# Kernel optimization log

Hardware: AMD Instinct MI355X
Metric: run time of the kernel (lower is better)

## Reference

```python
import jax, jax.numpy as jnp
import numpy as np

DEPTH = 7  # leaves = 2**(DEPTH-1) = 64

def setup_inputs() -> dict:
    key = jax.random.key(0)
    k1, k2, k3 = jax.random.split(key, 3)
    bs, dimx, dimy = 32768, 2048, 2048
    leaves = 2 ** (DEPTH - 1)
    x = jax.random.normal(k1, (bs, dimx), dtype=jnp.float32)
    w = 0.1 * jax.random.uniform(k2, (dimx, leaves - 1), dtype=jnp.float32)
    b = jnp.zeros((leaves - 1,), dtype=jnp.float32)
    responses = 0.1 * jax.random.uniform(k3, (leaves, dimy), dtype=jnp.float32)
    return {"x": x, "w": w, "b": b, "responses": responses}

def reference(x, w, b, responses):
    bs = x.shape[0]
    # gate probabilities for all internal nodes of the binary tree: [bs, leaves-1]
    gate = jax.nn.sigmoid(x @ w + b)
    running = jnp.ones((bs, 1), dtype=x.dtype)
    for i in range(1, DEPTH):
        parents = gate[:, 2 ** (i - 1) - 1: 2 ** i - 1]  # [bs, 2**(i-1)]
        # torch.stack([left, right], dim=1).reshape -> [left | right] concat order
        running = jnp.concatenate([parents * running, (1.0 - parents) * running], axis=1)
    return running @ responses  # [bs, dimy]
```

## Files before the change

### kernel.cpp

```cpp
#include <hip/hip_runtime.h>
#include <hip/hip_bf16.h>


typedef short bf16x8 __attribute__((ext_vector_type(8)));
typedef float f32x4  __attribute__((ext_vector_type(4)));

#define BS    32768
#define DIMX  2048
#define NODES 63
#define NL    64
#define DIMY  2048

__device__ __forceinline__ unsigned short f2bf(float f) {
    union { float f; unsigned int u; } v; v.f = f;
    unsigned int r = v.u + 0x7FFFu + ((v.u >> 16) & 1u);
    return (unsigned short)(r >> 16);
}
__device__ __forceinline__ float bf2f(unsigned short h) {
    union { float f; unsigned int u; } v; v.u = ((unsigned int)h) << 16;
    return v.f;
}

__global__ __launch_bounds__(256) void prep(const float* __restrict__ w,
                                            const float* __restrict__ R,
                                            unsigned short* __restrict__ wFs,
                                            unsigned short* __restrict__ RTs) {
    int f = blockIdx.x * 256 + threadIdx.x;
    if (f < 262144) {
        int e   = f & 7;
        int l   = (f >> 3) & 63;
        int hl  = (f >> 9) & 1;
        int g16 = (f >> 10) & 3;
        int kk  = (f >> 12) & 1;
        int k   = f >> 13;
        int n    = g16 * 16 + (l & 15);
        int kcol = k * 64 + kk * 32 + (l >> 4) * 8 + e;
        float v = (n < NODES) ? w[(size_t)kcol * NODES + n] : 0.0f;
        unsigned short h = f2bf(v);
        wFs[f] = hl ? f2bf(v - bf2f(h)) : h;
    } else {
        int f2 = f - 262144;
        int e  = f2 & 7;
        int l  = (f2 >> 3) & 63;
        int kh = (f2 >> 9) & 1;
        int nf = f2 >> 10;
        int k  = kh * 32 + (l >> 4) * 8 + e;
        int n  = nf * 16 + (l & 15);
        RTs[f2] = f2bf(R[(size_t)k * DIMY + n]);
    }
}

#define GBM   32
#define GBK   64
#define GLD   72
#define NSTEP (DIMX / GBK)

__device__ __forceinline__ bf16x8 pack8(float4 a, float4 b) {
    union { __hip_bfloat162 h2[4]; bf16x8 v; } u;
    u.h2[0] = __float22bfloat162_rn(make_float2(a.x, a.y));
    u.h2[1] = __float22bfloat162_rn(make_float2(a.z, a.w));
    u.h2[2] = __float22bfloat162_rn(make_float2(b.x, b.y));
    u.h2[3] = __float22bfloat162_rn(make_float2(b.z, b.w));
    return u.v;
}

__global__ __launch_bounds__(256, 6) void fused_kernel(const float* __restrict__ x,
                                                       const unsigned short* __restrict__ wFs,
                                                       const float* __restrict__ bias,
                                                       const unsigned short* __restrict__ RTs,
                                                       float* __restrict__ out) {
    __shared__ __align__(16) unsigned short xs[GBM][GLD];
    __shared__ float gl[GBM][NL + 1];

    const int t    = threadIdx.x;
    const int lane = t & 63;
    const int wv   = t >> 6;
    const int lr   = lane & 15;
    const int lg   = lane >> 4;
    const int m0   = blockIdx.x * GBM;
    const int rm   = wv & 1;
    const int cfp  = wv >> 1;

    const int xr = t >> 3;
    const int xc = (t & 7) * 8;
    const float* xsrc = x + (size_t)(m0 + xr) * DIMX + xc;

    const unsigned short* wb = wFs + (size_t)lane * 8;
    #define WFRAG(k, kk, ci, hl) \
        (*(const bf16x8*)(wb + (size_t)((((k) * 2 + (kk)) * 4 + (cfp * 2 + (ci))) * 2 + (hl)) * 512))

    float4 rx0 = *(const float4*)(xsrc);
    float4 rx1 = *(const float4*)(xsrc + 4);

    f32x4 acc[2];
    acc[0] = (f32x4){0.f, 0.f, 0.f, 0.f};
    acc[1] = (f32x4){0.f, 0.f, 0.f, 0.f};

    for (int k = 0; k < NSTEP; ++k) {
        __syncthreads();
        *(bf16x8*)&xs[xr][xc] = pack8(rx0, rx1);
        __syncthreads();
        if (k + 1 < NSTEP) {
            const int ko = (k + 1) * GBK;
            rx0 = *(const float4*)(xsrc + ko);
            rx1 = *(const float4*)(xsrc + ko + 4);
        }
        #pragma unroll
        for (int kk = 0; kk < 2; ++kk) {
            bf16x8 a = *(const bf16x8*)&xs[rm * 16 + lr][kk * 32 + lg * 8];
            #pragma unroll
            for (int ci = 0; ci < 2; ++ci) {
                bf16x8 bh = WFRAG(k, kk, ci, 0);
                bf16x8 bo = WFRAG(k, kk, ci, 1);
                acc[ci] = __builtin_amdgcn_mfma_f32_16x16x32_bf16(a, bh, acc[ci], 0, 0, 0);
                acc[ci] = __builtin_amdgcn_mfma_f32_16x16x32_bf16(a, bo, acc[ci], 0, 0, 0);
            }
        }
    }
    #undef WFRAG

    #pragma unroll
    for (int ci = 0; ci < 2; ++ci) {
        const int col = cfp * 32 + ci * 16 + lr;
        const float bb = bias[col < NODES ? col : 0];
        #pragma unroll
        for (int i = 0; i < 4; ++i) {
            int row = rm * 16 + lg * 4 + i;
            float s = acc[ci][i] + bb;
            gl[row][col] = 1.0f / (1.0f + __expf(-s));
        }
    }
    __syncthreads();

    {
        const int rr  = t >> 3;
        const int sub = t & 7;
        const int b5 = sub & 1, b4 = (sub >> 1) & 1, mh = sub >> 2;
        const float* g = gl[rr];
        float a2[2], a4[4], a8[8];
        float g0 = g[0];
        a2[0] = g0; a2[1] = 1.f - g0;
        #pragma unroll
        for (int m = 0; m < 4; ++m) {
            float gg = g[1 + (m & 1)];
            a4[m] = a2[m & 1] * ((m & 2) ? (1.f - gg) : gg);
        }
        #pragma unroll
        for (int m = 0; m < 8; ++m) {
            float gg = g[3 + (m & 3)];
            a8[m] = a4[m & 3] * ((m & 4) ? (1.f - gg) : gg);
        }
        unsigned short o[8];
        #pragma unroll
        for (int j = 0; j < 8; ++j) {
            int m = mh * 8 + j;
            float g4 = g[7 + j];
            float p  = a8[j] * (mh ? (1.f - g4) : g4);
            float g5 = g[15 + m];
            p *= b4 ? (1.f - g5) : g5;
            float g6 = g[31 + m + 16 * b4];
            p *= b5 ? (1.f - g6) : g6;
            o[j] = f2bf(p);
        }
        uint4 q;
        q.x = (unsigned)o[0] | ((unsigned)o[1] << 16);
        q.y = (unsigned)o[2] | ((unsigned)o[3] << 16);
        q.z = (unsigned)o[4] | ((unsigned)o[5] << 16);
        q.w = (unsigned)o[6] | ((unsigned)o[7] << 16);
        *(uint4*)&xs[rr][b5 * 32 + b4 * 16 + mh * 8] = q;
    }
    __syncthreads();

    bf16x8 pa[2][2];
    #pragma unroll
    for (int rf = 0; rf < 2; ++rf)
        #pragma unroll
        for (int kh = 0; kh < 2; ++kh)
            pa[rf][kh] = *(const bf16x8*)&xs[rf * 16 + lr][kh * 32 + lg * 8];

    const unsigned short* bbase = RTs + (size_t)(wv * 4) * 512 + (size_t)lane * 8;
    #define BLD(s, ci, kh) (*(const bf16x8*)(bbase + (size_t)(((s) * 16 + (ci) * 2 + (kh))) * 512))

    bf16x8 cur[4], nxt[4];
    cur[0] = BLD(0, 0, 0); cur[1] = BLD(0, 0, 1);
    cur[2] = BLD(0, 1, 0); cur[3] = BLD(0, 1, 1);

    float* op = out + (size_t)(m0 + lg * 4) * DIMY + wv * 32 + lr;

    #pragma unroll
    for (int s = 0; s < 16; ++s) {
        if (s + 1 < 16) {
            nxt[0] = BLD(s + 1, 0, 0); nxt[1] = BLD(s + 1, 0, 1);
            nxt[2] = BLD(s + 1, 1, 0); nxt[3] = BLD(s + 1, 1, 1);
        }
        f32x4 oa[2][2];
        #pragma unroll
        for (int rf = 0; rf < 2; ++rf)
            #pragma unroll
            for (int ci = 0; ci < 2; ++ci) {
                oa[rf][ci] = (f32x4){0.f, 0.f, 0.f, 0.f};
                oa[rf][ci] = __builtin_amdgcn_mfma_f32_16x16x32_bf16(pa[rf][0], cur[ci * 2 + 0],
                                                                     oa[rf][ci], 0, 0, 0);
                oa[rf][ci] = __builtin_amdgcn_mfma_f32_16x16x32_bf16(pa[rf][1], cur[ci * 2 + 1],
                                                                     oa[rf][ci], 0, 0, 0);
            }
        #pragma unroll
        for (int rf = 0; rf < 2; ++rf)
            #pragma unroll
            for (int ci = 0; ci < 2; ++ci)
                #pragma unroll
                for (int i = 0; i < 4; ++i)
                    op[(size_t)(rf * 16 + i) * DIMY + s * 128 + ci * 16] = oa[rf][ci][i];
        #pragma unroll
        for (int q = 0; q < 4; ++q) cur[q] = nxt[q];
    }
    #undef BLD
}

extern "C" void kernel_launch(void* const* d_in, const int* in_sizes, int n_in,
                              void* d_out, int out_size, void* d_ws, size_t ws_size,
                              hipStream_t stream) {
    const float* x = (const float*)d_in[0];
    const float* w = (const float*)d_in[1];
    const float* b = (const float*)d_in[2];
    const float* R = (const float*)d_in[3];
    float* out = (float*)d_out;

    char* ws = (char*)d_ws;
    unsigned short* wFs = (unsigned short*)ws;
    unsigned short* RTs = (unsigned short*)(ws + 524288);

    prep<<<dim3(1536), 256, 0, stream>>>(w, R, wFs, RTs);
    fused_kernel<<<dim3(BS / GBM), 256, 0, stream>>>(x, wFs, b, RTs, out);
}
```

Baseline: 155.7 us.

## Halve row tile to 16 per block and raise occupancy target

```diff
diff --git a/kernel.cpp b/kernel.cpp
--- a/kernel.cpp
+++ b/kernel.cpp
@@ -50,21 +50,12 @@
     }
 }
 
-#define GBM   32
+#define GBM   16
 #define GBK   64
 #define GLD   72
 #define NSTEP (DIMX / GBK)
 
-__device__ __forceinline__ bf16x8 pack8(float4 a, float4 b) {
-    union { __hip_bfloat162 h2[4]; bf16x8 v; } u;
-    u.h2[0] = __float22bfloat162_rn(make_float2(a.x, a.y));
-    u.h2[1] = __float22bfloat162_rn(make_float2(a.z, a.w));
-    u.h2[2] = __float22bfloat162_rn(make_float2(b.x, b.y));
-    u.h2[3] = __float22bfloat162_rn(make_float2(b.z, b.w));
-    return u.v;
-}
-
-__global__ __launch_bounds__(256, 6) void fused_kernel(const float* __restrict__ x,
+__global__ __launch_bounds__(256, 8) void fused_kernel(const float* __restrict__ x,
                                                        const unsigned short* __restrict__ wFs,
                                                        const float* __restrict__ bias,
                                                        const unsigned short* __restrict__ RTs,
@@ -78,64 +69,56 @@
     const int lr   = lane & 15;
     const int lg   = lane >> 4;
     const int m0   = blockIdx.x * GBM;
-    const int rm   = wv & 1;
-    const int cfp  = wv >> 1;
-
-    const int xr = t >> 3;
-    const int xc = (t & 7) * 8;
+
+    const int xr = t >> 4;
+    const int xc = (t & 15) * 4;
     const float* xsrc = x + (size_t)(m0 + xr) * DIMX + xc;
 
     const unsigned short* wb = wFs + (size_t)lane * 8;
-    #define WFRAG(k, kk, ci, hl) \
-        (*(const bf16x8*)(wb + (size_t)((((k) * 2 + (kk)) * 4 + (cfp * 2 + (ci))) * 2 + (hl)) * 512))
-
-    float4 rx0 = *(const float4*)(xsrc);
-    float4 rx1 = *(const float4*)(xsrc + 4);
-
-    f32x4 acc[2];
-    acc[0] = (f32x4){0.f, 0.f, 0.f, 0.f};
-    acc[1] = (f32x4){0.f, 0.f, 0.f, 0.f};
+    #define WFRAG(k, kk, hl) \
+        (*(const bf16x8*)(wb + (size_t)((((k) * 2 + (kk)) * 4 + wv) * 2 + (hl)) * 512))
+
+    float4 rx = *(const float4*)(xsrc);
+
+    f32x4 acc = (f32x4){0.f, 0.f, 0.f, 0.f};
 
     for (int k = 0; k < NSTEP; ++k) {
         __syncthreads();
-        *(bf16x8*)&xs[xr][xc] = pack8(rx0, rx1);
+        {
+            union { __hip_bfloat162 h2[2]; ushort4 v; } u;
+            u.h2[0] = __float22bfloat162_rn(make_float2(rx.x, rx.y));
+            u.h2[1] = __float22bfloat162_rn(make_float2(rx.z, rx.w));
+            *(ushort4*)&xs[xr][xc] = u.v;
+        }
         __syncthreads();
-        if (k + 1 < NSTEP) {
-            const int ko = (k + 1) * GBK;
-            rx0 = *(const float4*)(xsrc + ko);
-            rx1 = *(const float4*)(xsrc + ko + 4);
-        }
+        if (k + 1 < NSTEP)
+            rx = *(const float4*)(xsrc + (k + 1) * GBK);
         #pragma unroll
         for (int kk = 0; kk < 2; ++kk) {
-            bf16x8 a = *(const bf16x8*)&xs[rm * 16 + lr][kk * 32 + lg * 8];
-            #pragma unroll
-            for (int ci = 0; ci < 2; ++ci) {
-                bf16x8 bh = WFRAG(k, kk, ci, 0);
-                bf16x8 bo = WFRAG(k, kk, ci, 1);
-                acc[ci] = __builtin_amdgcn_mfma_f32_16x16x32_bf16(a, bh, acc[ci], 0, 0, 0);
-                acc[ci] = __builtin_amdgcn_mfma_f32_16x16x32_bf16(a, bo, acc[ci], 0, 0, 0);
-            }
+            bf16x8 a = *(const bf16x8*)&xs[lr][kk * 32 + lg * 8];
+            bf16x8 bh = WFRAG(k, kk, 0);
+            bf16x8 bo = WFRAG(k, kk, 1);
+            acc = __builtin_amdgcn_mfma_f32_16x16x32_bf16(a, bh, acc, 0, 0, 0);
+            acc = __builtin_amdgcn_mfma_f32_16x16x32_bf16(a, bo, acc, 0, 0, 0);
         }
     }
     #undef WFRAG
 
-    #pragma unroll
-    for (int ci = 0; ci < 2; ++ci) {
-        const int col = cfp * 32 + ci * 16 + lr;
+    {
+        const int col = wv * 16 + lr;
         const float bb = bias[col < NODES ? col : 0];
         #pragma unroll
         for (int i = 0; i < 4; ++i) {
-            int row = rm * 16 + lg * 4 + i;
-            float s = acc[ci][i] + bb;
-            gl[row][col] = 1.0f / (1.0f + __expf(-s));
+            float s = acc[i] + bb;
+            gl[lg * 4 + i][col] = 1.0f / (1.0f + __expf(-s));
         }
     }
     __syncthreads();
 
     {
-        const int rr  = t >> 3;
-        const int sub = t & 7;
-        const int b5 = sub & 1, b4 = (sub >> 1) & 1, mh = sub >> 2;
+        const int rr  = t >> 4;
+        const int sub = t & 15;
+        const int b5 = sub & 1, b4 = (sub >> 1) & 1, qq = sub >> 2;
         const float* g = gl[rr];
         float a2[2], a4[4], a8[8];
         float g0 = g[0];
@@ -150,69 +133,51 @@
             float gg = g[3 + (m & 3)];
             a8[m] = a4[m & 3] * ((m & 4) ? (1.f - gg) : gg);
         }
-        unsigned short o[8];
-        #pragma unroll
-        for (int j = 0; j < 8; ++j) {
-            int m = mh * 8 + j;
-            float g4 = g[7 + j];
-            float p  = a8[j] * (mh ? (1.f - g4) : g4);
+        unsigned short o[4];
+        #pragma unroll
+        for (int j = 0; j < 4; ++j) {
+            int m = qq * 4 + j;
+            float g4 = g[7 + (m & 7)];
+            float p  = a8[m & 7] * ((m & 8) ? (1.f - g4) : g4);
             float g5 = g[15 + m];
             p *= b4 ? (1.f - g5) : g5;
             float g6 = g[31 + m + 16 * b4];
             p *= b5 ? (1.f - g6) : g6;
             o[j] = f2bf(p);
         }
-        uint4 q;
-        q.x = (unsigned)o[0] | ((unsigned)o[1] << 16);
-        q.y = (unsigned)o[2] | ((unsigned)o[3] << 16);
-        q.z = (unsigned)o[4] | ((unsigned)o[5] << 16);
-        q.w = (unsigned)o[6] | ((unsigned)o[7] << 16);
-        *(uint4*)&xs[rr][b5 * 32 + b4 * 16 + mh * 8] = q;
+        uint2 qv;
+        qv.x = (unsigned)o[0] | ((unsigned)o[1] << 16);
+        qv.y = (unsigned)o[2] | ((unsigned)o[3] << 16);
+        *(uint2*)&xs[rr][b5 * 32 + b4 * 16 + qq * 4] = qv;
     }
     __syncthreads();
 
-    bf16x8 pa[2][2];
+    bf16x8 pa[2];
     #pragma unroll
-    for (int rf = 0; rf < 2; ++rf)
-        #pragma unroll
-        for (int kh = 0; kh < 2; ++kh)
-            pa[rf][kh] = *(const bf16x8*)&xs[rf * 16 + lr][kh * 32 + lg * 8];
-
-    const unsigned short* bbase = RTs + (size_t)(wv * 4) * 512 + (size_t)lane * 8;
-    #define BLD(s, ci, kh) (*(const bf16x8*)(bbase + (size_t)(((s) * 16 + (ci) * 2 + (kh))) * 512))
-
-    bf16x8 cur[4], nxt[4];
-    cur[0] = BLD(0, 0, 0); cur[1] = BLD(0, 0, 1);
-    cur[2] = BLD(0, 1, 0); cur[3] = BLD(0, 1, 1);
+    for (int kh = 0; kh < 2; ++kh)
+        pa[kh] = *(const bf16x8*)&xs[lr][kh * 32 + lg * 8];
+
+    const unsigned short* bbase = RTs + (size_t)lane * 8;
+    #define BLD(s, ci, kh) \
+        (*(const bf16x8*)(bbase + (size_t)((((s) * 8 + wv * 2 + (ci)) * 2 + (kh))) * 512))
 
     float* op = out + (size_t)(m0 + lg * 4) * DIMY + wv * 32 + lr;
 
     #pragma unroll
     for (int s = 0; s < 16; ++s) {
-        if (s + 1 < 16) {
-            nxt[0] = BLD(s + 1, 0, 0); nxt[1] = BLD(s + 1, 0, 1);
-            nxt[2] = BLD(s + 1, 1, 0); nxt[3] = BLD(s + 1, 1, 1);
-        }
-        f32x4 oa[2][2];
-        #pragma unroll
-        for (int rf = 0; rf < 2; ++rf)
-            #pragma unroll
-            for (int ci = 0; ci < 2; ++ci) {
-                oa[rf][ci] = (f32x4){0.f, 0.f, 0.f, 0.f};
-                oa[rf][ci] = __builtin_amdgcn_mfma_f32_16x16x32_bf16(pa[rf][0], cur[ci * 2 + 0],
-                                                                     oa[rf][ci], 0, 0, 0);
-                oa[rf][ci] = __builtin_amdgcn_mfma_f32_16x16x32_bf16(pa[rf][1], cur[ci * 2 + 1],
-                                                                     oa[rf][ci], 0, 0, 0);
-            }
-        #pragma unroll
-        for (int rf = 0; rf < 2; ++rf)
-            #pragma unroll
-            for (int ci = 0; ci < 2; ++ci)
-                #pragma unroll
-                for (int i = 0; i < 4; ++i)
-                    op[(size_t)(rf * 16 + i) * DIMY + s * 128 + ci * 16] = oa[rf][ci][i];
-        #pragma unroll
-        for (int q = 0; q < 4; ++q) cur[q] = nxt[q];
+        bf16x8 c00 = BLD(s, 0, 0), c01 = BLD(s, 0, 1);
+        bf16x8 c10 = BLD(s, 1, 0), c11 = BLD(s, 1, 1);
+        f32x4 oa0 = (f32x4){0.f, 0.f, 0.f, 0.f};
+        f32x4 oa1 = (f32x4){0.f, 0.f, 0.f, 0.f};
+        oa0 = __builtin_amdgcn_mfma_f32_16x16x32_bf16(pa[0], c00, oa0, 0, 0, 0);
+        oa0 = __builtin_amdgcn_mfma_f32_16x16x32_bf16(pa[1], c01, oa0, 0, 0, 0);
+        oa1 = __builtin_amdgcn_mfma_f32_16x16x32_bf16(pa[0], c10, oa1, 0, 0, 0);
+        oa1 = __builtin_amdgcn_mfma_f32_16x16x32_bf16(pa[1], c11, oa1, 0, 0, 0);
+        #pragma unroll
+        for (int i = 0; i < 4; ++i) {
+            op[(size_t)i * DIMY + s * 128]      = oa0[i];
+            op[(size_t)i * DIMY + s * 128 + 16] = oa1[i];
+        }
     }
     #undef BLD
 }
```

Measured after the change: 182.8 us. +17.4%, slower.
